# Kernel optimization log

Hardware: AMD Instinct MI355X
Metric: run time of the kernel (lower is better)

The kernel has to match this reference:

```python
import jax, jax.numpy as jnp
import numpy as np

B = 256        # trees per batch
DEPTH = 10     # complete binary tree depth -> 2^10 - 1 = 1023 internal nodes
N = 2**DEPTH - 1
IN = 128       # input_size
H = 128        # hidden_size
C = 5          # num_classes


def setup_inputs() -> dict:
    key = jax.random.key(0)
    ks = jax.random.split(key, 13)
    gdim = IN + 2 * H  # concat(x, h_left, h_right)
    inp = {"x": jax.random.normal(ks[0], (B, N, IN), jnp.float32)}
    names = ["i", "fl", "fr", "o", "u"]
    for j, nm in enumerate(names):
        inp[f"W_{nm}"] = 0.05 * jax.random.normal(ks[1 + 2 * j], (H, gdim), jnp.float32)
        inp[f"b_{nm}"] = 0.05 * jax.random.normal(ks[2 + 2 * j], (H,), jnp.float32)
    inp["W_cls"] = 0.05 * jax.random.normal(ks[11], (C, H), jnp.float32)
    inp["b_cls"] = 0.05 * jax.random.normal(ks[12], (C,), jnp.float32)
    return inp


def reference(x, W_i, b_i, W_fl, b_fl, W_fr, b_fr, W_o, b_o, W_u, b_u, W_cls, b_cls):
    # Level-order complete binary tree: node k has children 2k+1, 2k+2.
    # Bottom-up sweep; below the deepest internal level all children are
    # empty nodes with h = c = 0 (matches the original base case).
    Bb = x.shape[0]
    h = jnp.zeros((Bb, 2 ** DEPTH, H), x.dtype)
    c = jnp.zeros_like(h)
    for d in range(DEPTH - 1, -1, -1):  # fixed, small structural loop
        n = 2 ** d
        start = n - 1  # level-order offset of level d
        xs = x[:, start:start + n]            # [B, n, IN]
        hl, hr = h[:, 0::2], h[:, 1::2]       # children of node j are 2j, 2j+1 (level-local)
        cl, cr = c[:, 0::2], c[:, 1::2]
        comb = jnp.concatenate([xs, hl, hr], axis=-1)  # [B, n, IN+2H]
        lin = lambda W, b: jnp.einsum('bng,og->bno', comb, W) + b
        i = jax.nn.sigmoid(lin(W_i, b_i))
        fl = jax.nn.sigmoid(lin(W_fl, b_fl))
        fr = jax.nn.sigmoid(lin(W_fr, b_fr))
        o = jax.nn.sigmoid(lin(W_o, b_o))
        u = jnp.tanh(lin(W_u, b_u))
        c = i * u + fl * cl + fr * cr
        h = o * jnp.tanh(c)
    root_h = h[:, 0]                          # [B, H]
    logits = root_h @ W_cls.T + b_cls         # [B, C]
    return logits
```

## Files before the change

kernel.cpp:

```cpp
#include <hip/hip_runtime.h>
#include <hip/hip_bf16.h>
#include <stdint.h>


#define BATCH 256
#define NTOT 1023
#define HDIM 128
#define NCLS 5
#define GDIM 384

typedef __bf16 bf16x8 __attribute__((ext_vector_type(8)));
typedef float f32x4 __attribute__((ext_vector_type(4)));

__device__ __forceinline__ float sigmoid_f(float v) { return 1.f / (1.f + __expf(-v)); }
__device__ __forceinline__ float tanh_f(float v) { return 1.f - 2.f / (1.f + __expf(2.f * v)); }

__device__ __forceinline__ void load_lds16(const void* g, void* l) {
  __builtin_amdgcn_global_load_lds((const __attribute__((address_space(1))) unsigned int*)g,
                                   (__attribute__((address_space(3))) unsigned int*)l, 16, 0, 0);
}

__global__ __launch_bounds__(256) void pack_w(
    const float* __restrict__ W0, const float* __restrict__ W1, const float* __restrict__ W2,
    const float* __restrict__ W3, const float* __restrict__ W4, __bf16* __restrict__ PW)
{
  int t = blockIdx.x * 256 + threadIdx.x;
  int lane = t & 63;
  int chunk = t >> 6;
  int ks = chunk % 12;
  int jf = (chunk / 12) & 7;
  int g = chunk / 96;
  const float* W = (g == 0) ? W0 : (g == 1) ? W1 : (g == 2) ? W2 : (g == 3) ? W3 : W4;
  const float* s = W + (size_t)(jf * 16 + (lane & 15)) * GDIM + ks * 32 + (lane >> 4) * 8;
  float4 v0 = *(const float4*)s;
  float4 v1 = *(const float4*)(s + 4);
  bf16x8 w;
  w[0] = (__bf16)v0.x; w[1] = (__bf16)v0.y; w[2] = (__bf16)v0.z; w[3] = (__bf16)v0.w;
  w[4] = (__bf16)v1.x; w[5] = (__bf16)v1.y; w[6] = (__bf16)v1.z; w[7] = (__bf16)v1.w;
  *(bf16x8*)(PW + (size_t)t * 8) = w;
}

template<bool LEAF>
__device__ __forceinline__ void tile_body(
    const float* __restrict__ x, const __bf16* __restrict__ PW,
    const __bf16* __restrict__ h_prev, const float* __restrict__ c_prev,
    __bf16* __restrict__ h_out, float* __restrict__ c_out,
    const float* __restrict__ bv0, const float* __restrict__ bv1,
    const float* __restrict__ bv2, const float* __restrict__ bv3,
    const float* __restrict__ bv4,
    int d, int m0, int j0, unsigned char* lds)
{
  const int tid = threadIdx.x;
  const int w = tid >> 6;
  const int l = tid & 63;
  const int l15 = l & 15;
  const int quad = l >> 4;
  const int q8 = quad * 8;
  const int mh = w & 1, jh = w >> 1;
  const int n = 1 << d;
  const int jfb = j0 >> 4;
  constexpr int NKT = LEAF ? 4 : 12;
  constexpr int NBC = LEAF ? 3 : 5;

  const int ms = m0 + w * 16 + l15;
  const int bs = ms >> d;
  const int ids = ms & (n - 1);
  const float* xrow = x + ((size_t)bs * NTOT + (n - 1) + ids) * HDIM;
  const __bf16* hrow = LEAF ? (const __bf16*)nullptr
                            : h_prev + ((size_t)bs * 2 * n + 2 * ids) * HDIM;

  auto stage = [&](int ks) {
    unsigned char* Ab = lds + (ks & 1) * 24576;
    unsigned char* Bb = Ab + 4096;
#pragma unroll
    for (int q = 0; q < NBC; ++q) {
      int c = w * NBC + q;
      int g;
      if (LEAF) { const int gm[3] = {0, 3, 4}; g = gm[c >> 2]; }
      else g = c >> 2;
      int jfl = c & 3;
      const __bf16* s = PW + (((size_t)(g * 8 + jfb + jfl) * 12 + ks) * 64 + l) * 8;
      load_lds16(s, Bb + (g * 4 + jfl) * 1024);
    }
    if (LEAF || ks < 4) {
      const float* s = xrow + ks * 32 + q8;
      float4 v0 = *(const float4*)s;
      float4 v1 = *(const float4*)(s + 4);
      bf16x8 wv;
      wv[0] = (__bf16)v0.x; wv[1] = (__bf16)v0.y; wv[2] = (__bf16)v0.z; wv[3] = (__bf16)v0.w;
      wv[4] = (__bf16)v1.x; wv[5] = (__bf16)v1.y; wv[6] = (__bf16)v1.z; wv[7] = (__bf16)v1.w;
      *(bf16x8*)(Ab + w * 1024 + l * 16) = wv;
    } else {
      int off = (ks < 8) ? (ks - 4) * 32 : 128 + (ks - 8) * 32;
      load_lds16(hrow + off + q8, Ab + w * 1024);
    }
  };

  f32x4 acc[2][2][5];
#pragma unroll
  for (int mf = 0; mf < 2; ++mf)
#pragma unroll
    for (int jfl = 0; jfl < 2; ++jfl)
#pragma unroll
      for (int g = 0; g < 5; ++g)
        acc[mf][jfl][g] = (f32x4){0.f, 0.f, 0.f, 0.f};

  stage(0);
  for (int ks = 0; ks < NKT; ++ks) {
    __syncthreads();
    if (ks + 1 < NKT) stage(ks + 1);
    const unsigned char* Ab = lds + (ks & 1) * 24576;
    const unsigned char* Bb = Ab + 4096;
    bf16x8 a0 = *(const bf16x8*)(Ab + (mh * 2 + 0) * 1024 + l * 16);
    bf16x8 a1 = *(const bf16x8*)(Ab + (mh * 2 + 1) * 1024 + l * 16);
#pragma unroll
    for (int g = 0; g < 5; ++g) {
      if (LEAF && (g == 1 || g == 2)) continue;
#pragma unroll
      for (int jfl = 0; jfl < 2; ++jfl) {
        bf16x8 bb = *(const bf16x8*)(Bb + (g * 4 + jh * 2 + jfl) * 1024 + l * 16);
        acc[0][jfl][g] = __builtin_amdgcn_mfma_f32_16x16x32_bf16(a0, bb, acc[0][jfl][g], 0, 0, 0);
        acc[1][jfl][g] = __builtin_amdgcn_mfma_f32_16x16x32_bf16(a1, bb, acc[1][jfl][g], 0, 0, 0);
      }
    }
  }

#pragma unroll
  for (int jfl = 0; jfl < 2; ++jfl) {
    const int je = j0 + jh * 32 + jfl * 16 + l15;
    const float b0 = bv0[je], b1 = bv1[je], b2 = bv2[je], b3 = bv3[je], b4 = bv4[je];
#pragma unroll
    for (int mf = 0; mf < 2; ++mf) {
#pragma unroll
      for (int r = 0; r < 4; ++r) {
        int me = m0 + mh * 32 + mf * 16 + quad * 4 + r;
        int b = me >> d;
        int id = me & (n - 1);
        float gi = sigmoid_f(acc[mf][jfl][0][r] + b0);
        float go = sigmoid_f(acc[mf][jfl][3][r] + b3);
        float gu = tanh_f(acc[mf][jfl][4][r] + b4);
        float cv = gi * gu;
        if (!LEAF) {
          float gl = sigmoid_f(acc[mf][jfl][1][r] + b1);
          float gr = sigmoid_f(acc[mf][jfl][2][r] + b2);
          size_t cbase = ((size_t)b * 2 * n + 2 * id) * HDIM + je;
          cv += gl * c_prev[cbase] + gr * c_prev[cbase + HDIM];
        }
        size_t ob = ((size_t)b * n + id) * HDIM + je;
        c_out[ob] = cv;
        h_out[ob] = (__bf16)(go * tanh_f(cv));
      }
    }
  }
}

template<bool LEAF>
__global__ __launch_bounds__(256, 2) void level_kernel(
    const float* __restrict__ x, const __bf16* __restrict__ PW,
    const float* __restrict__ bv0, const float* __restrict__ bv1,
    const float* __restrict__ bv2, const float* __restrict__ bv3,
    const float* __restrict__ bv4,
    const __bf16* __restrict__ h_prev, const float* __restrict__ c_prev,
    __bf16* __restrict__ h_out, float* __restrict__ c_out, int d)
{
  __shared__ unsigned char lds[49152];
  tile_body<LEAF>(x, PW, h_prev, c_prev, h_out, c_out,
                  bv0, bv1, bv2, bv3, bv4, d,
                  (int)blockIdx.x * 64, (int)blockIdx.y * 64, lds);
}

#define TB_P  81920
#define TB_Q  132096
#define CSTR  132

__global__ __launch_bounds__(256, 1) void tail_kernel(
    const float* __restrict__ x, const __bf16* __restrict__ PW,
    const float* __restrict__ bv0, const float* __restrict__ bv1,
    const float* __restrict__ bv2, const float* __restrict__ bv3,
    const float* __restrict__ bv4,
    const float* __restrict__ Wcls, const float* __restrict__ bcls,
    const __bf16* __restrict__ h6, const float* __restrict__ c6,
    float* __restrict__ out)
{
  __shared__ unsigned char lds[157184];
  const int b = blockIdx.x;
  const int tid = threadIdx.x;
  const int w = tid >> 6;
  const int l = tid & 63;
  const int l15 = l & 15;
  const int quad = l >> 4;
  const int q8 = quad * 8;

  unsigned char* Ph = lds + TB_P;
  float* Pc = (float*)(lds + TB_P + 16384);
  unsigned char* Qh = lds + TB_Q;
  float* Qc = (float*)(lds + TB_Q + 8192);

  {
    const __bf16* hs = h6 + (size_t)b * 64 * HDIM;
#pragma unroll
    for (int it = 0; it < 4; ++it) {
      int idx = it * 256 + tid;
      int node = idx >> 4, i8 = idx & 15;
      bf16x8 v = *(const bf16x8*)(hs + node * HDIM + i8 * 8);
      *(bf16x8*)(Ph + node * 256 + ((i8 * 16) ^ ((node & 7) << 4))) = v;
    }
    const float* cs = c6 + (size_t)b * 64 * HDIM;
#pragma unroll
    for (int it = 0; it < 8; ++it) {
      int idx = it * 256 + tid;
      int node = idx >> 5, seg = idx & 31;
      float4 v = *(const float4*)(cs + node * HDIM + seg * 4);
      *(float4*)(Pc + node * CSTR + seg * 4) = v;
    }
  }

  for (int d = 5; d >= 0; --d) {
    const int s = 5 - d;
    const int n = 1 << d;
    const int nmf = (d == 5) ? 2 : 1;
    unsigned char* prev_h = (s & 1) ? Qh : Ph;
    float*         prev_c = (s & 1) ? Qc : Pc;
    unsigned char* cur_h  = (s & 1) ? Ph : Qh;
    float*         cur_c  = (s & 1) ? Pc : Qc;

    bf16x8 xf[2][4];
#pragma unroll
    for (int mf = 0; mf < 2; ++mf) {
      const float* xr = x + ((size_t)b * NTOT + (n - 1) + mf * 16 + l15) * HDIM + q8;
#pragma unroll
      for (int ks = 0; ks < 4; ++ks) {
        float4 v0 = *(const float4*)(xr + ks * 32);
        float4 v1 = *(const float4*)(xr + ks * 32 + 4);
        bf16x8 t;
        t[0] = (__bf16)v0.x; t[1] = (__bf16)v0.y; t[2] = (__bf16)v0.z; t[3] = (__bf16)v0.w;
        t[4] = (__bf16)v1.x; t[5] = (__bf16)v1.y; t[6] = (__bf16)v1.z; t[7] = (__bf16)v1.w;
        xf[mf][ks] = t;
      }
    }

    auto stageB = [&](int ks) {
      unsigned char* Bb = lds + (ks & 1) * 40960;
#pragma unroll
      for (int q = 0; q < 10; ++q) {
        int c = w * 10 + q;
        const __bf16* src = PW + ((size_t)(c * 12 + ks) * 64 + l) * 8;
        load_lds16(src, Bb + c * 1024);
      }
    };

    f32x4 acc[2][2][5];
#pragma unroll
    for (int mf = 0; mf < 2; ++mf)
#pragma unroll
      for (int jfl = 0; jfl < 2; ++jfl)
#pragma unroll
        for (int g = 0; g < 5; ++g)
          acc[mf][jfl][g] = (f32x4){0.f, 0.f, 0.f, 0.f};

    stageB(0);
    for (int ks = 0; ks < 12; ++ks) {
      __syncthreads();
      if (ks < 11) stageB(ks + 1);
      const unsigned char* Bb = lds + (ks & 1) * 40960;
      bf16x8 a0, a1;
      if (ks < 4) {
        a0 = xf[0][ks];
        a1 = xf[1][ks];
      } else {
        const int o = (ks < 8) ? 0 : 1;
        const int col2 = (((ks - (o ? 8 : 4)) * 32) + q8) * 2;
        int n0 = 2 * l15 + o;
        int n1 = 2 * (16 + l15) + o;
        a0 = *(const bf16x8*)(prev_h + n0 * 256 + (col2 ^ ((n0 & 7) << 4)));
        a1 = *(const bf16x8*)(prev_h + n1 * 256 + (col2 ^ ((n1 & 7) << 4)));
      }
#pragma unroll
      for (int g = 0; g < 5; ++g) {
#pragma unroll
        for (int jfl = 0; jfl < 2; ++jfl) {
          bf16x8 bb = *(const bf16x8*)(Bb + (g * 8 + w * 2 + jfl) * 1024 + l * 16);
          acc[0][jfl][g] = __builtin_amdgcn_mfma_f32_16x16x32_bf16(a0, bb, acc[0][jfl][g], 0, 0, 0);
          if (nmf == 2)
            acc[1][jfl][g] = __builtin_amdgcn_mfma_f32_16x16x32_bf16(a1, bb, acc[1][jfl][g], 0, 0, 0);
        }
      }
    }

#pragma unroll
    for (int jfl = 0; jfl < 2; ++jfl) {
      const int je = w * 32 + jfl * 16 + l15;
      const float b0 = bv0[je], b1 = bv1[je], b2 = bv2[je], b3 = bv3[je], b4 = bv4[je];
#pragma unroll
      for (int mf = 0; mf < 2; ++mf) {
#pragma unroll
        for (int r = 0; r < 4; ++r) {
          const int me = mf * 16 + quad * 4 + r;
          if (me < n) {
            float gi = sigmoid_f(acc[mf][jfl][0][r] + b0);
            float gl = sigmoid_f(acc[mf][jfl][1][r] + b1);
            float gr = sigmoid_f(acc[mf][jfl][2][r] + b2);
            float go = sigmoid_f(acc[mf][jfl][3][r] + b3);
            float gu = tanh_f(acc[mf][jfl][4][r] + b4);
            float cv = gi * gu + gl * prev_c[(2 * me) * CSTR + je]
                               + gr * prev_c[(2 * me + 1) * CSTR + je];
            cur_c[me * CSTR + je] = cv;
            *(__bf16*)(cur_h + me * 256 + ((je * 2) ^ ((me & 7) << 4))) =
                (__bf16)(go * tanh_f(cv));
          }
        }
      }
    }
  }

  __syncthreads();
  if (tid < NCLS) {
    float sacc = bcls[tid];
    for (int k = 0; k < HDIM; ++k)
      sacc += (float)(*(const __bf16*)(Ph + k * 2)) * Wcls[tid * HDIM + k];
    out[(size_t)b * NCLS + tid] = sacc;
  }
}

extern "C" void kernel_launch(void* const* d_in, const int* in_sizes, int n_in,
                              void* d_out, int out_size, void* d_ws, size_t ws_size,
                              hipStream_t stream) {
  const float* x  = (const float*)d_in[0];
  const float* W[5]  = {(const float*)d_in[1], (const float*)d_in[3], (const float*)d_in[5],
                        (const float*)d_in[7], (const float*)d_in[9]};
  const float* bv[5] = {(const float*)d_in[2], (const float*)d_in[4], (const float*)d_in[6],
                        (const float*)d_in[8], (const float*)d_in[10]};
  const float* Wcls = (const float*)d_in[11];
  const float* bcls = (const float*)d_in[12];

  uint8_t* ws = (uint8_t*)d_ws;
  __bf16* hb0 = (__bf16*)ws;
  __bf16* hb1 = (__bf16*)(ws + 33554432);
  float*  cb0 = (float*)(ws + 50331648);
  float*  cb1 = (float*)(ws + 117440512);
  __bf16* PW  = (__bf16*)(ws + 150994944);

  pack_w<<<120, 256, 0, stream>>>(W[0], W[1], W[2], W[3], W[4], PW);

  level_kernel<true><<<dim3(2048, 2), 256, 0, stream>>>(
      x, PW, bv[0], bv[1], bv[2], bv[3], bv[4], hb1, cb1, hb0, cb0, 9);
  for (int d = 8; d >= 6; --d) {
    const int p = 9 - d;
    __bf16* h_out = (p & 1) ? hb1 : hb0;
    float*  c_out = (p & 1) ? cb1 : cb0;
    const __bf16* h_prev = (p & 1) ? hb0 : hb1;
    const float*  c_prev = (p & 1) ? cb0 : cb1;
    dim3 grid((BATCH << d) >> 6, 2);
    level_kernel<false><<<grid, 256, 0, stream>>>(
        x, PW, bv[0], bv[1], bv[2], bv[3], bv[4], h_prev, c_prev, h_out, c_out, d);
  }
  tail_kernel<<<BATCH, 256, 0, stream>>>(
      x, PW, bv[0], bv[1], bv[2], bv[3], bv[4],
      Wcls, bcls, hb1, cb1, (float*)d_out);
}
```

Before: 457.3 us.

## Shrink leaf LDS and accumulators, prefetch child cell state, raise occupancy

For the leaf level, the B tiles are packed contiguously so only the three needed gates use LDS. This cuts leaf LDS to 32KB and leaf accumulators to three gate sets. Launch bounds rise to 4 blocks per CU for leaves and 3 for internal levels. Child cell states are loaded into registers before the K loop so their latency overlaps the MFMA work. The added register pressure from the prefetch and the tighter launch bounds could cause spills.

```diff
diff --git a/kernel.cpp b/kernel.cpp
--- a/kernel.cpp
+++ b/kernel.cpp
@@ -61,6 +61,10 @@
   const int jfb = j0 >> 4;
   constexpr int NKT = LEAF ? 4 : 12;
   constexpr int NBC = LEAF ? 3 : 5;
+  constexpr int NACC = LEAF ? 3 : 5;
+  constexpr int BUFS = LEAF ? 16384 : 24576;
+  constexpr int AI_O = LEAF ? 1 : 3;
+  constexpr int AI_U = LEAF ? 2 : 4;
 
   const int ms = m0 + w * 16 + l15;
   const int bs = ms >> d;
@@ -69,8 +73,28 @@
   const __bf16* hrow = LEAF ? (const __bf16*)nullptr
                             : h_prev + ((size_t)bs * 2 * n + 2 * ids) * HDIM;
 
+  float cpl[2][2][4], cpr[2][2][4];
+  if constexpr (!LEAF) {
+#pragma unroll
+    for (int jfl = 0; jfl < 2; ++jfl) {
+      const int je = j0 + jh * 32 + jfl * 16 + l15;
+#pragma unroll
+      for (int mf = 0; mf < 2; ++mf) {
+#pragma unroll
+        for (int r = 0; r < 4; ++r) {
+          const int me = m0 + mh * 32 + mf * 16 + quad * 4 + r;
+          const int bb_ = me >> d;
+          const int id = me & (n - 1);
+          const size_t cbase = ((size_t)bb_ * 2 * n + 2 * id) * HDIM + je;
+          cpl[jfl][mf][r] = c_prev[cbase];
+          cpr[jfl][mf][r] = c_prev[cbase + HDIM];
+        }
+      }
+    }
+  }
+
   auto stage = [&](int ks) {
-    unsigned char* Ab = lds + (ks & 1) * 24576;
+    unsigned char* Ab = lds + (ks & 1) * BUFS;
     unsigned char* Bb = Ab + 4096;
 #pragma unroll
     for (int q = 0; q < NBC; ++q) {
@@ -80,7 +104,7 @@
       else g = c >> 2;
       int jfl = c & 3;
       const __bf16* s = PW + (((size_t)(g * 8 + jfb + jfl) * 12 + ks) * 64 + l) * 8;
-      load_lds16(s, Bb + (g * 4 + jfl) * 1024);
+      load_lds16(s, Bb + c * 1024);
     }
     if (LEAF || ks < 4) {
       const float* s = xrow + ks * 32 + q8;
@@ -96,31 +120,30 @@
     }
   };
 
-  f32x4 acc[2][2][5];
+  f32x4 acc[2][2][NACC];
 #pragma unroll
   for (int mf = 0; mf < 2; ++mf)
 #pragma unroll
     for (int jfl = 0; jfl < 2; ++jfl)
 #pragma unroll
-      for (int g = 0; g < 5; ++g)
-        acc[mf][jfl][g] = (f32x4){0.f, 0.f, 0.f, 0.f};
+      for (int ai = 0; ai < NACC; ++ai)
+        acc[mf][jfl][ai] = (f32x4){0.f, 0.f, 0.f, 0.f};
 
   stage(0);
   for (int ks = 0; ks < NKT; ++ks) {
     __syncthreads();
     if (ks + 1 < NKT) stage(ks + 1);
-    const unsigned char* Ab = lds + (ks & 1) * 24576;
+    const unsigned char* Ab = lds + (ks & 1) * BUFS;
     const unsigned char* Bb = Ab + 4096;
     bf16x8 a0 = *(const bf16x8*)(Ab + (mh * 2 + 0) * 1024 + l * 16);
     bf16x8 a1 = *(const bf16x8*)(Ab + (mh * 2 + 1) * 1024 + l * 16);
 #pragma unroll
-    for (int g = 0; g < 5; ++g) {
-      if (LEAF && (g == 1 || g == 2)) continue;
+    for (int ai = 0; ai < NACC; ++ai) {
 #pragma unroll
       for (int jfl = 0; jfl < 2; ++jfl) {
-        bf16x8 bb = *(const bf16x8*)(Bb + (g * 4 + jh * 2 + jfl) * 1024 + l * 16);
-        acc[0][jfl][g] = __builtin_amdgcn_mfma_f32_16x16x32_bf16(a0, bb, acc[0][jfl][g], 0, 0, 0);
-        acc[1][jfl][g] = __builtin_amdgcn_mfma_f32_16x16x32_bf16(a1, bb, acc[1][jfl][g], 0, 0, 0);
+        bf16x8 bb = *(const bf16x8*)(Bb + (ai * 4 + jh * 2 + jfl) * 1024 + l * 16);
+        acc[0][jfl][ai] = __builtin_amdgcn_mfma_f32_16x16x32_bf16(a0, bb, acc[0][jfl][ai], 0, 0, 0);
+        acc[1][jfl][ai] = __builtin_amdgcn_mfma_f32_16x16x32_bf16(a1, bb, acc[1][jfl][ai], 0, 0, 0);
       }
     }
   }
@@ -128,7 +151,7 @@
 #pragma unroll
   for (int jfl = 0; jfl < 2; ++jfl) {
     const int je = j0 + jh * 32 + jfl * 16 + l15;
-    const float b0 = bv0[je], b1 = bv1[je], b2 = bv2[je], b3 = bv3[je], b4 = bv4[je];
+    const float b0 = bv0[je], b3 = bv3[je], b4 = bv4[je];
 #pragma unroll
     for (int mf = 0; mf < 2; ++mf) {
 #pragma unroll
@@ -137,14 +160,13 @@
         int b = me >> d;
         int id = me & (n - 1);
         float gi = sigmoid_f(acc[mf][jfl][0][r] + b0);
-        float go = sigmoid_f(acc[mf][jfl][3][r] + b3);
-        float gu = tanh_f(acc[mf][jfl][4][r] + b4);
+        float go = sigmoid_f(acc[mf][jfl][AI_O][r] + b3);
+        float gu = tanh_f(acc[mf][jfl][AI_U][r] + b4);
         float cv = gi * gu;
-        if (!LEAF) {
-          float gl = sigmoid_f(acc[mf][jfl][1][r] + b1);
-          float gr = sigmoid_f(acc[mf][jfl][2][r] + b2);
-          size_t cbase = ((size_t)b * 2 * n + 2 * id) * HDIM + je;
-          cv += gl * c_prev[cbase] + gr * c_prev[cbase + HDIM];
+        if constexpr (!LEAF) {
+          float gl = sigmoid_f(acc[mf][jfl][1][r] + bv1[je]);
+          float gr = sigmoid_f(acc[mf][jfl][2][r] + bv2[je]);
+          cv += gl * cpl[jfl][mf][r] + gr * cpr[jfl][mf][r];
         }
         size_t ob = ((size_t)b * n + id) * HDIM + je;
         c_out[ob] = cv;
@@ -155,7 +177,7 @@
 }
 
 template<bool LEAF>
-__global__ __launch_bounds__(256, 2) void level_kernel(
+__global__ __launch_bounds__(256, (LEAF ? 4 : 3)) void level_kernel(
     const float* __restrict__ x, const __bf16* __restrict__ PW,
     const float* __restrict__ bv0, const float* __restrict__ bv1,
     const float* __restrict__ bv2, const float* __restrict__ bv3,
@@ -163,7 +185,7 @@
     const __bf16* __restrict__ h_prev, const float* __restrict__ c_prev,
     __bf16* __restrict__ h_out, float* __restrict__ c_out, int d)
 {
-  __shared__ unsigned char lds[49152];
+  __shared__ unsigned char lds[LEAF ? 32768 : 49152];
   tile_body<LEAF>(x, PW, h_prev, c_prev, h_out, c_out,
                   bv0, bv1, bv2, bv3, bv4, d,
                   (int)blockIdx.x * 64, (int)blockIdx.y * 64, lds);
```

New measurement: 463.5 us. No clear change (+1.4%).

## Shrink level tiles to 64x32, load A fragments directly into registers

Applied to the files above, without the earlier changes.

The level kernels now use a 64-row by 32-column output tile per block, with each wave owning 16 rows and all 32 columns. The A operand (x and child h rows) is read straight from global memory into registers instead of being staged through LDS, and the h-part is consumed first so the x loads overlap. Only weights are double-buffered in LDS, which cuts shared memory per block and lets more blocks fit per CU. The cost is twice as many blocks, each re-reading x and h rows for its column slice, and less weight reuse per block.

```diff
diff --git a/kernel.cpp b/kernel.cpp
--- a/kernel.cpp
+++ b/kernel.cpp
@@ -40,6 +40,8 @@
   *(bf16x8*)(PW + (size_t)t * 8) = w;
 }
 
+__constant__ int GM_LEAF[3] = {0, 3, 4};
+
 template<bool LEAF>
 __device__ __forceinline__ void tile_body(
     const float* __restrict__ x, const __bf16* __restrict__ PW,
@@ -56,106 +58,111 @@
   const int l15 = l & 15;
   const int quad = l >> 4;
   const int q8 = quad * 8;
-  const int mh = w & 1, jh = w >> 1;
   const int n = 1 << d;
   const int jfb = j0 >> 4;
+  constexpr int NACC = LEAF ? 3 : 5;
+  constexpr int NCH = 2 * NACC;
+  constexpr int BUFS = NCH * 1024;
   constexpr int NKT = LEAF ? 4 : 12;
-  constexpr int NBC = LEAF ? 3 : 5;
 
   const int ms = m0 + w * 16 + l15;
   const int bs = ms >> d;
   const int ids = ms & (n - 1);
-  const float* xrow = x + ((size_t)bs * NTOT + (n - 1) + ids) * HDIM;
-  const __bf16* hrow = LEAF ? (const __bf16*)nullptr
-                            : h_prev + ((size_t)bs * 2 * n + 2 * ids) * HDIM;
-
-  auto stage = [&](int ks) {
-    unsigned char* Ab = lds + (ks & 1) * 24576;
-    unsigned char* Bb = Ab + 4096;
-#pragma unroll
-    for (int q = 0; q < NBC; ++q) {
-      int c = w * NBC + q;
-      int g;
-      if (LEAF) { const int gm[3] = {0, 3, 4}; g = gm[c >> 2]; }
-      else g = c >> 2;
-      int jfl = c & 3;
-      const __bf16* s = PW + (((size_t)(g * 8 + jfb + jfl) * 12 + ks) * 64 + l) * 8;
-      load_lds16(s, Bb + (g * 4 + jfl) * 1024);
-    }
-    if (LEAF || ks < 4) {
-      const float* s = xrow + ks * 32 + q8;
-      float4 v0 = *(const float4*)s;
-      float4 v1 = *(const float4*)(s + 4);
-      bf16x8 wv;
-      wv[0] = (__bf16)v0.x; wv[1] = (__bf16)v0.y; wv[2] = (__bf16)v0.z; wv[3] = (__bf16)v0.w;
-      wv[4] = (__bf16)v1.x; wv[5] = (__bf16)v1.y; wv[6] = (__bf16)v1.z; wv[7] = (__bf16)v1.w;
-      *(bf16x8*)(Ab + w * 1024 + l * 16) = wv;
-    } else {
-      int off = (ks < 8) ? (ks - 4) * 32 : 128 + (ks - 8) * 32;
-      load_lds16(hrow + off + q8, Ab + w * 1024);
+  const float* xr = x + ((size_t)bs * NTOT + (n - 1) + ids) * HDIM + q8;
+  const __bf16* hr = LEAF ? (const __bf16*)nullptr
+                          : h_prev + ((size_t)bs * 2 * n + 2 * ids) * HDIM + q8;
+
+  auto stageB = [&](int t, int wks) {
+    unsigned char* Bb = lds + (t & 1) * BUFS;
+#pragma unroll
+    for (int q = 0; q < 3; ++q) {
+      int c = w + q * 4;
+      if (c < NCH) {
+        int ai = c >> 1, jfl = c & 1;
+        int g = LEAF ? GM_LEAF[ai] : ai;
+        const __bf16* src = PW + (((size_t)(g * 8 + jfb + jfl) * 12 + wks) * 64 + l) * 8;
+        load_lds16(src, Bb + c * 1024);
+      }
     }
   };
 
-  f32x4 acc[2][2][5];
-#pragma unroll
-  for (int mf = 0; mf < 2; ++mf)
-#pragma unroll
-    for (int jfl = 0; jfl < 2; ++jfl)
-#pragma unroll
-      for (int g = 0; g < 5; ++g)
-        acc[mf][jfl][g] = (f32x4){0.f, 0.f, 0.f, 0.f};
-
-  stage(0);
-  for (int ks = 0; ks < NKT; ++ks) {
+  stageB(0, LEAF ? 0 : 4);
+
+  bf16x8 xf[4];
+#pragma unroll
+  for (int kx = 0; kx < 4; ++kx) {
+    float4 v0 = *(const float4*)(xr + kx * 32);
+    float4 v1 = *(const float4*)(xr + kx * 32 + 4);
+    bf16x8 t;
+    t[0] = (__bf16)v0.x; t[1] = (__bf16)v0.y; t[2] = (__bf16)v0.z; t[3] = (__bf16)v0.w;
+    t[4] = (__bf16)v1.x; t[5] = (__bf16)v1.y; t[6] = (__bf16)v1.z; t[7] = (__bf16)v1.w;
+    xf[kx] = t;
+  }
+
+  bf16x8 ah[2];
+  if constexpr (!LEAF) ah[0] = *(const bf16x8*)(hr);
+
+  f32x4 acc[2][NACC];
+#pragma unroll
+  for (int jfl = 0; jfl < 2; ++jfl)
+#pragma unroll
+    for (int ai = 0; ai < NACC; ++ai)
+      acc[jfl][ai] = (f32x4){0.f, 0.f, 0.f, 0.f};
+
+#pragma unroll
+  for (int t = 0; t < NKT; ++t) {
     __syncthreads();
-    if (ks + 1 < NKT) stage(ks + 1);
-    const unsigned char* Ab = lds + (ks & 1) * 24576;
-    const unsigned char* Bb = Ab + 4096;
-    bf16x8 a0 = *(const bf16x8*)(Ab + (mh * 2 + 0) * 1024 + l * 16);
-    bf16x8 a1 = *(const bf16x8*)(Ab + (mh * 2 + 1) * 1024 + l * 16);
-#pragma unroll
-    for (int g = 0; g < 5; ++g) {
-      if (LEAF && (g == 1 || g == 2)) continue;
+    if (t + 1 < NKT) {
+      stageB(t + 1, LEAF ? (t + 1) : ((t + 5) % 12));
+      if constexpr (!LEAF) {
+        if (t + 1 < 8) {
+          const int o = ((t + 1) < 4) ? 0 : 1;
+          ah[(t + 1) & 1] = *(const bf16x8*)(hr + o * HDIM + ((t + 1) & 3) * 32);
+        }
+      }
+    }
+    bf16x8 a;
+    if constexpr (LEAF) a = xf[t];
+    else a = (t < 8) ? ah[t & 1] : xf[t - 8];
+    const unsigned char* Bb = lds + (t & 1) * BUFS;
+#pragma unroll
+    for (int ai = 0; ai < NACC; ++ai) {
 #pragma unroll
       for (int jfl = 0; jfl < 2; ++jfl) {
-        bf16x8 bb = *(const bf16x8*)(Bb + (g * 4 + jh * 2 + jfl) * 1024 + l * 16);
-        acc[0][jfl][g] = __builtin_amdgcn_mfma_f32_16x16x32_bf16(a0, bb, acc[0][jfl][g], 0, 0, 0);
-        acc[1][jfl][g] = __builtin_amdgcn_mfma_f32_16x16x32_bf16(a1, bb, acc[1][jfl][g], 0, 0, 0);
+        bf16x8 bb = *(const bf16x8*)(Bb + (ai * 2 + jfl) * 1024 + l * 16);
+        acc[jfl][ai] = __builtin_amdgcn_mfma_f32_16x16x32_bf16(a, bb, acc[jfl][ai], 0, 0, 0);
       }
     }
   }
 
 #pragma unroll
   for (int jfl = 0; jfl < 2; ++jfl) {
-    const int je = j0 + jh * 32 + jfl * 16 + l15;
-    const float b0 = bv0[je], b1 = bv1[je], b2 = bv2[je], b3 = bv3[je], b4 = bv4[je];
-#pragma unroll
-    for (int mf = 0; mf < 2; ++mf) {
-#pragma unroll
-      for (int r = 0; r < 4; ++r) {
-        int me = m0 + mh * 32 + mf * 16 + quad * 4 + r;
-        int b = me >> d;
-        int id = me & (n - 1);
-        float gi = sigmoid_f(acc[mf][jfl][0][r] + b0);
-        float go = sigmoid_f(acc[mf][jfl][3][r] + b3);
-        float gu = tanh_f(acc[mf][jfl][4][r] + b4);
-        float cv = gi * gu;
-        if (!LEAF) {
-          float gl = sigmoid_f(acc[mf][jfl][1][r] + b1);
-          float gr = sigmoid_f(acc[mf][jfl][2][r] + b2);
-          size_t cbase = ((size_t)b * 2 * n + 2 * id) * HDIM + je;
-          cv += gl * c_prev[cbase] + gr * c_prev[cbase + HDIM];
-        }
-        size_t ob = ((size_t)b * n + id) * HDIM + je;
-        c_out[ob] = cv;
-        h_out[ob] = (__bf16)(go * tanh_f(cv));
-      }
+    const int je = j0 + jfl * 16 + l15;
+    const float b0 = bv0[je], b3 = bv3[je], b4 = bv4[je];
+#pragma unroll
+    for (int r = 0; r < 4; ++r) {
+      const int me = m0 + w * 16 + quad * 4 + r;
+      const int b = me >> d;
+      const int id = me & (n - 1);
+      float gi = sigmoid_f(acc[jfl][0][r] + b0);
+      float go = sigmoid_f(acc[jfl][LEAF ? 1 : 3][r] + b3);
+      float gu = tanh_f(acc[jfl][LEAF ? 2 : 4][r] + b4);
+      float cv = gi * gu;
+      if constexpr (!LEAF) {
+        float gl = sigmoid_f(acc[jfl][1][r] + bv1[je]);
+        float gr = sigmoid_f(acc[jfl][2][r] + bv2[je]);
+        size_t cbase = ((size_t)b * 2 * n + 2 * id) * HDIM + je;
+        cv += gl * c_prev[cbase] + gr * c_prev[cbase + HDIM];
+      }
+      size_t ob = ((size_t)b * n + id) * HDIM + je;
+      c_out[ob] = cv;
+      h_out[ob] = (__bf16)(go * tanh_f(cv));
     }
   }
 }
 
 template<bool LEAF>
-__global__ __launch_bounds__(256, 2) void level_kernel(
+__global__ __launch_bounds__(256, (LEAF ? 5 : 4)) void level_kernel(
     const float* __restrict__ x, const __bf16* __restrict__ PW,
     const float* __restrict__ bv0, const float* __restrict__ bv1,
     const float* __restrict__ bv2, const float* __restrict__ bv3,
@@ -163,10 +170,10 @@
     const __bf16* __restrict__ h_prev, const float* __restrict__ c_prev,
     __bf16* __restrict__ h_out, float* __restrict__ c_out, int d)
 {
-  __shared__ unsigned char lds[49152];
+  __shared__ unsigned char lds[LEAF ? 12288 : 20480];
   tile_body<LEAF>(x, PW, h_prev, c_prev, h_out, c_out,
                   bv0, bv1, bv2, bv3, bv4, d,
-                  (int)blockIdx.x * 64, (int)blockIdx.y * 64, lds);
+                  (int)blockIdx.x * 64, (int)blockIdx.y * 32, lds);
 }
 
 #define TB_P  81920
@@ -342,7 +349,7 @@
 
   pack_w<<<120, 256, 0, stream>>>(W[0], W[1], W[2], W[3], W[4], PW);
 
-  level_kernel<true><<<dim3(2048, 2), 256, 0, stream>>>(
+  level_kernel<true><<<dim3(2048, 4), 256, 0, stream>>>(
       x, PW, bv[0], bv[1], bv[2], bv[3], bv[4], hb1, cb1, hb0, cb0, 9);
   for (int d = 8; d >= 6; --d) {
     const int p = 9 - d;
@@ -350,7 +357,7 @@
     float*  c_out = (p & 1) ? cb1 : cb0;
     const __bf16* h_prev = (p & 1) ? hb0 : hb1;
     const float*  c_prev = (p & 1) ? cb0 : cb1;
-    dim3 grid((BATCH << d) >> 6, 2);
+    dim3 grid((BATCH << d) >> 6, 4);
     level_kernel<false><<<grid, 256, 0, stream>>>(
         x, PW, bv[0], bv[1], bv[2], bv[3], bv[4], h_prev, c_prev, h_out, c_out, d);
   }
```

After: 486.0 us. 1.06x slower.
